# Kernel optimization log

Measured on AMD Instinct MI355X. Metric: run time of the kernel, lower is better.

The kernel has to match this reference:

```python
import jax, jax.numpy as jnp
import numpy as np
import math

B, T, D, H = 4, 2048, 512, 8
DK = D // H


def setup_inputs() -> dict:
    key = jax.random.key(0)
    ks = jax.random.split(key, 12)
    s = 0.02
    return {
        "query": jax.random.normal(ks[0], (B, T, D), jnp.float32),
        "key": jax.random.normal(ks[1], (B, T, D), jnp.float32),
        "value": jax.random.normal(ks[2], (B, T, D), jnp.float32),
        "mask": jnp.ones((B, T), jnp.int32),
        "Wq": jax.random.normal(ks[3], (D, D), jnp.float32) * s,
        "bq": jax.random.normal(ks[4], (D,), jnp.float32) * s,
        "Wk": jax.random.normal(ks[5], (D, D), jnp.float32) * s,
        "bk": jax.random.normal(ks[6], (D,), jnp.float32) * s,
        "Wv": jax.random.normal(ks[7], (D, D), jnp.float32) * s,
        "bv": jax.random.normal(ks[8], (D,), jnp.float32) * s,
        "Wo": jax.random.normal(ks[9], (D, D), jnp.float32) * s,
        "bo": jax.random.normal(ks[10], (D,), jnp.float32) * s,
    }


def _split_heads(x):
    # [B,T,D] -> [B,H,T,DK]
    return x.reshape(B, T, H, DK).transpose(0, 2, 1, 3)


def reference(query, key, value, mask, Wq, bq, Wk, bk, Wv, bv, Wo, bo):
    # torch Linear: y = x @ W.T + b
    q = _split_heads(query @ Wq.T + bq)
    k = _split_heads(key @ Wk.T + bk)
    v = _split_heads(value @ Wv.T + bv)
    scores = jnp.einsum("bhqd,bhkd->bhqk", q, k) / math.sqrt(DK)
    m = mask[:, None, None, :]  # [B,1,1,T] broadcast over heads and query pos
    scores = jnp.where(m == 0, jnp.float32(-1e9), scores)
    p_attn = jax.nn.softmax(scores, axis=-1)
    sigmoid_p_attn = jax.nn.sigmoid(scores)
    # dropout omitted (deterministic eval reference)
    x = jnp.einsum("bhqk,bhkd->bhqd", p_attn, v)
    x = x.transpose(0, 2, 1, 3).reshape(B, T, D)
    out = x @ Wo.T + bo
    return out, sigmoid_p_attn
```

## Files before the change

kernel.cpp:

```cpp
#include <hip/hip_runtime.h>
#include <hip/hip_bf16.h>


#define DEV static __device__ __forceinline__

typedef __attribute__((ext_vector_type(8))) short bf16x8;
typedef __attribute__((ext_vector_type(4))) float f32x4;

constexpr int BB = 4, TT = 2048, DD = 512, HH = 8, DKK = 64;

DEV short f2bf(float f) {
  unsigned u = __float_as_uint(f);
  unsigned r = 0x7fffu + ((u >> 16) & 1u);
  return (short)((u + r) >> 16);
}

template <bool A_IS_BF16, bool OUT_BF16>
DEV void gemm_body(const void* Av, const float* __restrict__ W,
                   const float* __restrict__ bias, void* Cv,
                   short (*As)[72], short (*Ws)[72]) {
  const int tid = threadIdx.x;
  const int lane = tid & 63;
  const int wv = tid >> 6;
  const int wm = wv >> 1, wn = wv & 1;
  const int m0 = blockIdx.x * 128;
  const int n0 = blockIdx.y * 128;
  const int K = 512;
  const int l15 = lane & 15, l4 = lane >> 4;

  f32x4 acc[4][4] = {};

  for (int kk = 0; kk < K; kk += 64) {
    __syncthreads();
    if constexpr (!A_IS_BF16) {
      const float* A = (const float*)Av;
#pragma unroll
      for (int r2 = 0; r2 < 8; ++r2) {
        int idx = r2 * 256 + tid;
        int row = idx >> 4, c4 = idx & 15;
        float4 v = *(const float4*)&A[(size_t)(m0 + row) * K + kk + c4 * 4];
        union { short h[4]; unsigned long long u; } cv;
        cv.h[0] = f2bf(v.x); cv.h[1] = f2bf(v.y);
        cv.h[2] = f2bf(v.z); cv.h[3] = f2bf(v.w);
        *(unsigned long long*)&As[row][c4 * 4] = cv.u;
      }
    } else {
      const short* A = (const short*)Av;
#pragma unroll
      for (int r2 = 0; r2 < 4; ++r2) {
        int idx = r2 * 256 + tid;
        int row = idx >> 3, c8 = idx & 7;
        *(bf16x8*)&As[row][c8 * 8] =
            *(const bf16x8*)&A[(size_t)(m0 + row) * K + kk + c8 * 8];
      }
    }
#pragma unroll
    for (int r2 = 0; r2 < 8; ++r2) {
      int idx = r2 * 256 + tid;
      int row = idx >> 4, c4 = idx & 15;
      float4 v = *(const float4*)&W[(size_t)(n0 + row) * K + kk + c4 * 4];
      union { short h[4]; unsigned long long u; } cv;
      cv.h[0] = f2bf(v.x); cv.h[1] = f2bf(v.y);
      cv.h[2] = f2bf(v.z); cv.h[3] = f2bf(v.w);
      *(unsigned long long*)&Ws[row][c4 * 4] = cv.u;
    }
    __syncthreads();

#pragma unroll
    for (int kf = 0; kf < 2; ++kf) {
      bf16x8 af[4], bf[4];
#pragma unroll
      for (int i = 0; i < 4; ++i)
        af[i] = *(const bf16x8*)&As[wm * 64 + i * 16 + l15][kf * 32 + l4 * 8];
#pragma unroll
      for (int j = 0; j < 4; ++j)
        bf[j] = *(const bf16x8*)&Ws[wn * 64 + j * 16 + l15][kf * 32 + l4 * 8];
#pragma unroll
      for (int i = 0; i < 4; ++i)
#pragma unroll
        for (int j = 0; j < 4; ++j)
          acc[i][j] = __builtin_amdgcn_mfma_f32_16x16x32_bf16(af[i], bf[j],
                                                              acc[i][j], 0, 0, 0);
    }
  }

#pragma unroll
  for (int i = 0; i < 4; ++i) {
    int rbase = m0 + wm * 64 + i * 16 + l4 * 4;
#pragma unroll
    for (int j = 0; j < 4; ++j) {
      int col = n0 + wn * 64 + j * 16 + l15;
      float bv = bias[col];
#pragma unroll
      for (int rg = 0; rg < 4; ++rg) {
        float val = acc[i][j][rg] + bv;
        size_t off = (size_t)(rbase + rg) * 512 + col;
        if constexpr (OUT_BF16)
          ((short*)Cv)[off] = f2bf(val);
        else
          ((float*)Cv)[off] = val;
      }
    }
  }
}

struct ProjArgs {
  const float* A[3];
  const float* W[3];
  const float* bias[3];
  short* C[3];
};

__global__ __launch_bounds__(256)
void proj_gemm_kernel(ProjArgs args) {
  __shared__ short As[128][72];
  __shared__ short Ws[128][72];
  const int z = blockIdx.z;
  gemm_body<false, true>(args.A[z], args.W[z], args.bias[z], args.C[z], As, Ws);
}

__global__ __launch_bounds__(256)
void out_gemm_kernel(const short* __restrict__ X, const float* __restrict__ W,
                     const float* __restrict__ bias, float* __restrict__ C) {
  __shared__ short As[128][72];
  __shared__ short Ws[128][72];
  gemm_body<true, false>(X, W, bias, C, As, Ws);
}

__global__ __launch_bounds__(256)
void attn_kernel(const short* __restrict__ Qp, const short* __restrict__ Kp,
                 const short* __restrict__ Vp, const int* __restrict__ mask,
                 float* __restrict__ sig, short* __restrict__ Xout) {
  __shared__ short Kt[64][72];
  __shared__ short Vt[64][72];
  __shared__ short Pl[4][16][72];

  const int tid = threadIdx.x;
  const int lane = tid & 63;
  const int w = tid >> 6;
  const int q0 = blockIdx.x * 64;
  const int h = blockIdx.y;
  const int b = blockIdx.z;
  const int l15 = lane & 15, l4 = lane >> 4;

  bf16x8 qf[2];
  {
    const short* qptr = &Qp[((size_t)b * TT + q0 + w * 16 + l15) * DD + h * DKK];
    qf[0] = *(const bf16x8*)&qptr[l4 * 8];
    qf[1] = *(const bf16x8*)&qptr[32 + l4 * 8];
  }

  float m_r[4], l_r[4];
  f32x4 accO[4] = {};
#pragma unroll
  for (int i = 0; i < 4; ++i) { m_r[i] = -INFINITY; l_r[i] = 0.f; }

  for (int kv0 = 0; kv0 < TT; kv0 += 64) {
    __syncthreads();
#pragma unroll
    for (int r2 = 0; r2 < 2; ++r2) {
      int idx = r2 * 256 + tid;
      int kr = idx >> 3, c8 = idx & 7;
      *(bf16x8*)&Kt[kr][c8 * 8] =
          *(const bf16x8*)&Kp[((size_t)b * TT + kv0 + kr) * DD + h * DKK + c8 * 8];
    }
#pragma unroll
    for (int r2 = 0; r2 < 2; ++r2) {
      int idx = r2 * 256 + tid;
      int kv = idx & 63, c8 = idx >> 6;
      bf16x8 vv = *(const bf16x8*)&Vp[((size_t)b * TT + kv0 + kv) * DD + h * DKK + c8 * 8];
#pragma unroll
      for (int i = 0; i < 8; ++i) Vt[c8 * 8 + i][kv] = vv[i];
    }
    __syncthreads();

    f32x4 s[4] = {};
#pragma unroll
    for (int kf = 0; kf < 2; ++kf) {
#pragma unroll
      for (int j = 0; j < 4; ++j) {
        bf16x8 kb = *(const bf16x8*)&Kt[j * 16 + l15][kf * 32 + l4 * 8];
        s[j] = __builtin_amdgcn_mfma_f32_16x16x32_bf16(qf[kf], kb, s[j], 0, 0, 0);
      }
    }

    int mv[4];
#pragma unroll
    for (int j = 0; j < 4; ++j) mv[j] = mask[b * TT + kv0 + j * 16 + l15];
#pragma unroll
    for (int j = 0; j < 4; ++j)
#pragma unroll
      for (int i = 0; i < 4; ++i) {
        float sv = s[j][i] * 0.125f;
        s[j][i] = (mv[j] == 0) ? -1.0e9f : sv;
      }

    float tm[4], mn[4], cor[4], em[4];
#pragma unroll
    for (int i = 0; i < 4; ++i) {
      tm[i] = fmaxf(fmaxf(s[0][i], s[1][i]), fmaxf(s[2][i], s[3][i]));
#pragma unroll
      for (int d = 1; d < 16; d <<= 1) tm[i] = fmaxf(tm[i], __shfl_xor(tm[i], d));
      mn[i] = fmaxf(m_r[i], tm[i]);
      cor[i] = __expf(m_r[i] - mn[i]);
      em[i] = __expf(-mn[i]);
    }

    float rs[4] = {0.f, 0.f, 0.f, 0.f};
#pragma unroll
    for (int j = 0; j < 4; ++j)
#pragma unroll
      for (int i = 0; i < 4; ++i) {
        float p = __expf(s[j][i] - mn[i]);
        float sg = p * __builtin_amdgcn_rcpf(p + em[i]);
        size_t soff = (((size_t)(b * HH + h)) * TT + (q0 + w * 16 + l4 * 4 + i)) * TT
                      + kv0 + j * 16 + l15;
        sig[soff] = sg;
        rs[i] += p;
        Pl[w][l4 * 4 + i][j * 16 + l15] = f2bf(p);
      }
#pragma unroll
    for (int i = 0; i < 4; ++i) {
#pragma unroll
      for (int d = 1; d < 16; d <<= 1) rs[i] += __shfl_xor(rs[i], d);
      l_r[i] = l_r[i] * cor[i] + rs[i];
      m_r[i] = mn[i];
    }
#pragma unroll
    for (int n = 0; n < 4; ++n)
#pragma unroll
      for (int i = 0; i < 4; ++i) accO[n][i] *= cor[i];

    __syncthreads();

    bf16x8 pa0 = *(const bf16x8*)&Pl[w][l15][l4 * 8];
    bf16x8 pa1 = *(const bf16x8*)&Pl[w][l15][32 + l4 * 8];
#pragma unroll
    for (int n = 0; n < 4; ++n) {
      bf16x8 vb0 = *(const bf16x8*)&Vt[n * 16 + l15][l4 * 8];
      bf16x8 vb1 = *(const bf16x8*)&Vt[n * 16 + l15][32 + l4 * 8];
      accO[n] = __builtin_amdgcn_mfma_f32_16x16x32_bf16(pa0, vb0, accO[n], 0, 0, 0);
      accO[n] = __builtin_amdgcn_mfma_f32_16x16x32_bf16(pa1, vb1, accO[n], 0, 0, 0);
    }
  }

#pragma unroll
  for (int i = 0; i < 4; ++i) {
    float inv = __builtin_amdgcn_rcpf(l_r[i]);
#pragma unroll
    for (int n = 0; n < 4; ++n) {
      Xout[((size_t)b * TT + q0 + w * 16 + l4 * 4 + i) * DD + h * DKK + n * 16 + l15] =
          f2bf(accO[n][i] * inv);
    }
  }
}

extern "C" void kernel_launch(void* const* d_in, const int* in_sizes, int n_in,
                              void* d_out, int out_size, void* d_ws, size_t ws_size,
                              hipStream_t stream) {
  const float* query = (const float*)d_in[0];
  const float* key   = (const float*)d_in[1];
  const float* value = (const float*)d_in[2];
  const int*   mask  = (const int*)d_in[3];
  const float* Wq = (const float*)d_in[4];
  const float* bq = (const float*)d_in[5];
  const float* Wk = (const float*)d_in[6];
  const float* bk = (const float*)d_in[7];
  const float* Wv = (const float*)d_in[8];
  const float* bv = (const float*)d_in[9];
  const float* Wo = (const float*)d_in[10];
  const float* bo = (const float*)d_in[11];

  const size_t NTOK = (size_t)BB * TT * DD;
  short* Qp = (short*)d_ws;
  short* Kp = Qp + NTOK;
  short* Vp = Kp + NTOK;
  short* Xx = Vp + NTOK;

  float* outp = (float*)d_out;
  float* sig  = outp + NTOK;

  ProjArgs pa;
  pa.A[0] = query; pa.A[1] = key; pa.A[2] = value;
  pa.W[0] = Wq; pa.W[1] = Wk; pa.W[2] = Wv;
  pa.bias[0] = bq; pa.bias[1] = bk; pa.bias[2] = bv;
  pa.C[0] = Qp; pa.C[1] = Kp; pa.C[2] = Vp;

  dim3 g1(64, 4, 3);
  proj_gemm_kernel<<<g1, 256, 0, stream>>>(pa);

  dim3 g2(TT / 64, HH, BB);
  attn_kernel<<<g2, 256, 0, stream>>>(Qp, Kp, Vp, mask, sig, Xx);

  dim3 g3(64, 4, 1);
  out_gemm_kernel<<<g3, 256, 0, stream>>>(Xx, Wo, bo, outp);
}
```

Measured before the change: 743.4 us.

## Split sigmoid score output into a dedicated kernel with coalesced stores

Moves the sigmoid-of-scores output into a separate kernel. That kernel recomputes QK^T per tile, stages the results through shared memory and writes them as float4 row-contiguous stores, replacing the scattered 4-byte stores that were interleaved with the softmax loop. The attention kernel now only computes the softmax-weighted output, reads K fragments directly from global memory instead of through shared memory, and drops one barrier. The trade-off is a redundant QK^T computation and an extra kernel launch in exchange for better store coalescing and a lighter main loop.

```diff
diff --git a/kernel.cpp b/kernel.cpp
--- a/kernel.cpp
+++ b/kernel.cpp
@@ -128,10 +128,68 @@
 }
 
 __global__ __launch_bounds__(256)
+void sig_kernel(const short* __restrict__ Qp, const short* __restrict__ Kp,
+                const int* __restrict__ mask, float* __restrict__ sig) {
+  __shared__ float Tr[4][16][72];
+
+  const int tid = threadIdx.x;
+  const int lane = tid & 63;
+  const int w = tid >> 6;
+  const int l15 = lane & 15, l4 = lane >> 4;
+  const int kv0 = blockIdx.x * 128;
+  const int q0 = blockIdx.y * 64;
+  const int bh = blockIdx.z;
+  const int b = bh >> 3, h = bh & 7;
+
+  const short* qrow = &Qp[((size_t)b * TT + q0 + w * 16 + l15) * DD + h * DKK];
+  bf16x8 qf0 = *(const bf16x8*)&qrow[l4 * 8];
+  bf16x8 qf1 = *(const bf16x8*)&qrow[32 + l4 * 8];
+
+  size_t obase = ((size_t)bh * TT + q0 + w * 16) * TT + kv0;
+
+#pragma unroll
+  for (int ch = 0; ch < 2; ++ch) {
+    f32x4 s[4];
+#pragma unroll
+    for (int j = 0; j < 4; ++j) {
+      const short* krow =
+          &Kp[((size_t)b * TT + kv0 + ch * 64 + j * 16 + l15) * DD + h * DKK];
+      bf16x8 kb0 = *(const bf16x8*)&krow[l4 * 8];
+      bf16x8 kb1 = *(const bf16x8*)&krow[32 + l4 * 8];
+      f32x4 z = {};
+      z = __builtin_amdgcn_mfma_f32_16x16x32_bf16(qf0, kb0, z, 0, 0, 0);
+      s[j] = __builtin_amdgcn_mfma_f32_16x16x32_bf16(qf1, kb1, z, 0, 0, 0);
+    }
+#pragma unroll
+    for (int j = 0; j < 4; ++j) {
+      int mv = mask[b * TT + kv0 + ch * 64 + j * 16 + l15];
+#pragma unroll
+      for (int i = 0; i < 4; ++i) {
+        float sv = s[j][i] * 0.125f;
+        float sg = (mv == 0)
+                       ? 0.f
+                       : __builtin_amdgcn_rcpf(1.f + __expf(-sv));
+        Tr[w][l4 * 4 + i][j * 16 + l15] = sg;
+      }
+    }
+    asm volatile("s_waitcnt lgkmcnt(0)" ::: "memory");
+    __builtin_amdgcn_sched_barrier(0);
+#pragma unroll
+    for (int s4 = 0; s4 < 4; ++s4) {
+      float4 vv = *(const float4*)&Tr[w][s4 * 4 + l4][l15 * 4];
+      *(float4*)&sig[obase + (size_t)(s4 * 4 + l4) * TT + ch * 64 + l15 * 4] = vv;
+    }
+    if (ch == 0) {
+      asm volatile("s_waitcnt lgkmcnt(0)" ::: "memory");
+      __builtin_amdgcn_sched_barrier(0);
+    }
+  }
+}
+
+__global__ __launch_bounds__(256)
 void attn_kernel(const short* __restrict__ Qp, const short* __restrict__ Kp,
                  const short* __restrict__ Vp, const int* __restrict__ mask,
-                 float* __restrict__ sig, short* __restrict__ Xout) {
-  __shared__ short Kt[64][72];
+                 short* __restrict__ Xout) {
   __shared__ short Vt[64][72];
   __shared__ short Pl[4][16][72];
 
@@ -160,28 +218,20 @@
 #pragma unroll
     for (int r2 = 0; r2 < 2; ++r2) {
       int idx = r2 * 256 + tid;
-      int kr = idx >> 3, c8 = idx & 7;
-      *(bf16x8*)&Kt[kr][c8 * 8] =
-          *(const bf16x8*)&Kp[((size_t)b * TT + kv0 + kr) * DD + h * DKK + c8 * 8];
-    }
-#pragma unroll
-    for (int r2 = 0; r2 < 2; ++r2) {
-      int idx = r2 * 256 + tid;
       int kv = idx & 63, c8 = idx >> 6;
       bf16x8 vv = *(const bf16x8*)&Vp[((size_t)b * TT + kv0 + kv) * DD + h * DKK + c8 * 8];
 #pragma unroll
       for (int i = 0; i < 8; ++i) Vt[c8 * 8 + i][kv] = vv[i];
     }
-    __syncthreads();
 
     f32x4 s[4] = {};
 #pragma unroll
-    for (int kf = 0; kf < 2; ++kf) {
-#pragma unroll
-      for (int j = 0; j < 4; ++j) {
-        bf16x8 kb = *(const bf16x8*)&Kt[j * 16 + l15][kf * 32 + l4 * 8];
-        s[j] = __builtin_amdgcn_mfma_f32_16x16x32_bf16(qf[kf], kb, s[j], 0, 0, 0);
-      }
+    for (int j = 0; j < 4; ++j) {
+      const short* krow = &Kp[((size_t)b * TT + kv0 + j * 16 + l15) * DD + h * DKK];
+      bf16x8 kb0 = *(const bf16x8*)&krow[l4 * 8];
+      bf16x8 kb1 = *(const bf16x8*)&krow[32 + l4 * 8];
+      s[j] = __builtin_amdgcn_mfma_f32_16x16x32_bf16(qf[0], kb0, s[j], 0, 0, 0);
+      s[j] = __builtin_amdgcn_mfma_f32_16x16x32_bf16(qf[1], kb1, s[j], 0, 0, 0);
     }
 
     int mv[4];
@@ -195,7 +245,7 @@
         s[j][i] = (mv[j] == 0) ? -1.0e9f : sv;
       }
 
-    float tm[4], mn[4], cor[4], em[4];
+    float tm[4], mn[4], cor[4];
 #pragma unroll
     for (int i = 0; i < 4; ++i) {
       tm[i] = fmaxf(fmaxf(s[0][i], s[1][i]), fmaxf(s[2][i], s[3][i]));
@@ -203,7 +253,6 @@
       for (int d = 1; d < 16; d <<= 1) tm[i] = fmaxf(tm[i], __shfl_xor(tm[i], d));
       mn[i] = fmaxf(m_r[i], tm[i]);
       cor[i] = __expf(m_r[i] - mn[i]);
-      em[i] = __expf(-mn[i]);
     }
 
     float rs[4] = {0.f, 0.f, 0.f, 0.f};
@@ -212,10 +261,6 @@
 #pragma unroll
       for (int i = 0; i < 4; ++i) {
         float p = __expf(s[j][i] - mn[i]);
-        float sg = p * __builtin_amdgcn_rcpf(p + em[i]);
-        size_t soff = (((size_t)(b * HH + h)) * TT + (q0 + w * 16 + l4 * 4 + i)) * TT
-                      + kv0 + j * 16 + l15;
-        sig[soff] = sg;
         rs[i] += p;
         Pl[w][l4 * 4 + i][j * 16 + l15] = f2bf(p);
       }
@@ -289,8 +334,11 @@
   dim3 g1(64, 4, 3);
   proj_gemm_kernel<<<g1, 256, 0, stream>>>(pa);
 
+  dim3 gs(TT / 128, TT / 64, BB * HH);
+  sig_kernel<<<gs, 256, 0, stream>>>(Qp, Kp, mask, sig);
+
   dim3 g2(TT / 64, HH, BB);
-  attn_kernel<<<g2, 256, 0, stream>>>(Qp, Kp, Vp, mask, sig, Xx);
+  attn_kernel<<<g2, 256, 0, stream>>>(Qp, Kp, Vp, mask, Xx);
 
   dim3 g3(64, 4, 1);
   out_gemm_kernel<<<g3, 256, 0, stream>>>(Xx, Wo, bo, outp);
```

Result: slower. 907.7 us (+22.1%).
